# Optimization experiments

Hardware: AMD Instinct MI355X
Metric: run time of the kernel (lower is better)

Reference implementation:

```python
import jax, jax.numpy as jnp
import numpy as np


def _pos_encoding(seq_length: int, d_model: int, dtype):
    # wave[j] = 10000 ** (j / d_model) for every dim index j (pairs share base exponent pattern)
    j = jnp.arange(d_model, dtype=dtype)
    wave = jnp.power(jnp.asarray(10000.0, dtype), j / d_model)  # [d_model]
    pos = jnp.arange(seq_length, dtype=dtype)                    # [S]
    angles = pos[:, None] / wave[None, :]                        # [S, d_model]
    even = (jnp.arange(d_model) % 2) == 0
    return jnp.where(even[None, :], jnp.sin(angles), jnp.cos(angles))


def setup_inputs() -> dict:
    key = jax.random.key(0)
    x = jax.random.normal(key, (8, 4096, 1024), dtype=jnp.float32)
    return {"x": x}


def reference(x) -> jnp.ndarray:
    B, S, D = x.shape
    pe = _pos_encoding(S, D, x.dtype)  # [S, D], broadcast over batch
    return x + pe[None, :, :]
```

## Files before the change

kernel.cpp:

```cpp
#include <hip/hip_runtime.h>
#include <math.h>

constexpr int B = 8;
constexpr int S = 4096;
constexpr int D = 1024;
constexpr int DQ = D / 4;
constexpr int DQ_SHIFT = 8;
constexpr int PLANE4 = S * DQ;

#define NEG_L2_10000_OVER_D (-13.287712379549449f / 1024.0f)

__global__ __launch_bounds__(256)
void pe_add_kernel(const float* __restrict__ x, float* __restrict__ out) {
    const int idx4 = blockIdx.x * blockDim.x + threadIdx.x;
    if (idx4 >= PLANE4) return;

    const int dq = idx4 & (DQ - 1);
    const int s  = idx4 >> DQ_SHIFT;
    const int d0 = dq << 2;

    const float fs = (float)s;

    const float a0 = fs * exp2f((float)(d0 + 0) * NEG_L2_10000_OVER_D);
    const float a1 = fs * exp2f((float)(d0 + 1) * NEG_L2_10000_OVER_D);
    const float a2 = fs * exp2f((float)(d0 + 2) * NEG_L2_10000_OVER_D);
    const float a3 = fs * exp2f((float)(d0 + 3) * NEG_L2_10000_OVER_D);

    float4 pe;
    pe.x = sinf(a0);
    pe.y = cosf(a1);
    pe.z = sinf(a2);
    pe.w = cosf(a3);

    const float4* __restrict__ xv = (const float4*)x;
    float4* __restrict__ ov = (float4*)out;

#pragma unroll
    for (int b = 0; b < B; ++b) {
        const size_t off = (size_t)b * PLANE4 + idx4;
        float4 v = xv[off];
        v.x += pe.x;
        v.y += pe.y;
        v.z += pe.z;
        v.w += pe.w;
        ov[off] = v;
    }
}

extern "C" void kernel_launch(void* const* d_in, const int* in_sizes, int n_in,
                              void* d_out, int out_size, void* d_ws, size_t ws_size,
                              hipStream_t stream) {
    const float* x = (const float*)d_in[0];
    float* out = (float*)d_out;

    const int threads = 256;
    const int blocks = (PLANE4 + threads - 1) / threads;
    pe_add_kernel<<<blocks, threads, 0, stream>>>(x, out);
}
```

Measured before the change: 243.0 us.

## Flatten grid to one float4 per thread and use fast sin/cos intrinsics

Each thread now handles a single float4 of the full batch tensor and recomputes its positional-encoding values, instead of computing them once and looping over the 8 batches. This trades 8x more transcendental work for far more threads in flight, which should keep more memory requests outstanding on a purely bandwidth-bound op. Precise sinf/cosf are replaced by the __sinf/__cosf intrinsics to keep that extra trig work cheap. The risk is accuracy: angles reach several thousand radians, where the fast hardware sine and cosine can drift from the reference.

```diff
diff --git a/kernel.cpp b/kernel.cpp
--- a/kernel.cpp
+++ b/kernel.cpp
@@ -7,44 +7,35 @@
 constexpr int DQ = D / 4;
 constexpr int DQ_SHIFT = 8;
 constexpr int PLANE4 = S * DQ;
+constexpr int TOTAL4 = B * PLANE4;
 
 #define NEG_L2_10000_OVER_D (-13.287712379549449f / 1024.0f)
 
 __global__ __launch_bounds__(256)
 void pe_add_kernel(const float* __restrict__ x, float* __restrict__ out) {
     const int idx4 = blockIdx.x * blockDim.x + threadIdx.x;
-    if (idx4 >= PLANE4) return;
 
-    const int dq = idx4 & (DQ - 1);
-    const int s  = idx4 >> DQ_SHIFT;
-    const int d0 = dq << 2;
+    const float4* __restrict__ xv = (const float4*)x;
+    float4* __restrict__ ov = (float4*)out;
+    float4 v = xv[idx4];
+
+    const int pidx = idx4 & (PLANE4 - 1);
+    const int dq   = pidx & (DQ - 1);
+    const int s    = pidx >> DQ_SHIFT;
+    const int d0   = dq << 2;
 
     const float fs = (float)s;
-
     const float a0 = fs * exp2f((float)(d0 + 0) * NEG_L2_10000_OVER_D);
     const float a1 = fs * exp2f((float)(d0 + 1) * NEG_L2_10000_OVER_D);
     const float a2 = fs * exp2f((float)(d0 + 2) * NEG_L2_10000_OVER_D);
     const float a3 = fs * exp2f((float)(d0 + 3) * NEG_L2_10000_OVER_D);
 
-    float4 pe;
-    pe.x = sinf(a0);
-    pe.y = cosf(a1);
-    pe.z = sinf(a2);
-    pe.w = cosf(a3);
+    v.x += __sinf(a0);
+    v.y += __cosf(a1);
+    v.z += __sinf(a2);
+    v.w += __cosf(a3);
 
-    const float4* __restrict__ xv = (const float4*)x;
-    float4* __restrict__ ov = (float4*)out;
-
-#pragma unroll
-    for (int b = 0; b < B; ++b) {
-        const size_t off = (size_t)b * PLANE4 + idx4;
-        float4 v = xv[off];
-        v.x += pe.x;
-        v.y += pe.y;
-        v.z += pe.z;
-        v.w += pe.w;
-        ov[off] = v;
-    }
+    ov[idx4] = v;
 }
 
 extern "C" void kernel_launch(void* const* d_in, const int* in_sizes, int n_in,
@@ -54,6 +45,6 @@
     float* out = (float*)d_out;
 
     const int threads = 256;
-    const int blocks = (PLANE4 + threads - 1) / threads;
+    const int blocks = TOTAL4 / threads;
     pe_add_kernel<<<blocks, threads, 0, stream>>>(x, out);
 }
```

Result: faster. 219.3 us (-9.8%).
